# Kernel tuning notes

Measured on AMD Instinct MI355X. Metric: run time of the kernel, lower is better.

## Reference

```python
import jax, jax.numpy as jnp
import numpy as np
from jax import lax

K = 20
SLOPE = 0.01


def setup_inputs() -> dict:
    key = jax.random.key(0)
    k1, k2 = jax.random.split(key)
    x = jax.random.normal(k1, (8, 64, 4096), dtype=jnp.float32)
    # Conv2d(2*64, 64, kernel_size=1, bias=False) weight, squeezed to (out, in)
    W = jax.random.normal(k2, (64, 128), dtype=jnp.float32) * 0.05
    return {"x": x, "W": W}


def reference(x, W):
    # x: (B, C, N), W: (O, 2C)
    B, C, N = x.shape
    # --- knn: pairwise_distance[b,i,j] = -||x_i||^2 + 2 x_i.x_j - ||x_j||^2 ---
    xx = jnp.sum(x * x, axis=1)                      # (B, N)
    inner = jnp.einsum('bcn,bcm->bnm', x, x)         # (B, N, N)
    pdist = 2.0 * inner - xx[:, :, None] - xx[:, None, :]
    idx = lax.top_k(pdist, K)[1]                     # (B, N, K) neighbor indices
    # --- get_graph_feature: gather neighbors, diff + center concat ---
    x_t = jnp.transpose(x, (0, 2, 1))                # (B, N, C)
    neigh = x_t[jnp.arange(B)[:, None, None], idx]   # (B, N, K, C)
    center = x_t[:, :, None, :]                      # (B, N, 1, C)
    feat = jnp.concatenate(
        [neigh - center, jnp.broadcast_to(center, (B, N, K, C))], axis=-1
    )                                                # (B, N, K, 2C)
    # --- 1x1 conv (no bias) + LeakyReLU ---
    h = jnp.einsum('bnkd,od->bonk', feat, W)         # (B, O, N, K)
    h = jnp.where(h >= 0, h, SLOPE * h)
    # --- max over neighbors ---
    return jnp.max(h, axis=-1)                       # (B, O, N)
```

## Files before the change

### kernel.cpp

```cpp
#include <hip/hip_runtime.h>
#include <cfloat>

#define B_ 8
#define C_ 64
#define N_ 4096
#define K_ 20
#define MARGIN 0.08f
#define CAP 64

typedef float f32x4v  __attribute__((ext_vector_type(4)));
typedef float f32x16v __attribute__((ext_vector_type(16)));
typedef _Float16 f16x8 __attribute__((ext_vector_type(8)));
typedef unsigned long long u64;

#define OFF_IDX 131072
#define OFF_QG  2752512
#define OFF_P0  19529728
#define OFF_P1  23724032

__global__ __launch_bounds__(256) void k_split(const float* __restrict__ x,
                                               unsigned short* __restrict__ p0,
                                               unsigned short* __restrict__ p1,
                                               float* __restrict__ xxn) {
    int b = blockIdx.x & 7, mt = blockIdx.x >> 3;
    int m = mt * 256 + threadIdx.x;
    const float* xb = x + (size_t)b * C_ * N_;
    double ss = 0.0;
#pragma unroll 1
    for (int seg = 0; seg < 8; ++seg) {
        unsigned short h0[8], h1[8];
#pragma unroll
        for (int j = 0; j < 8; ++j) {
            float v = xb[(size_t)(seg * 8 + j) * N_ + m];
            ss += (double)v * (double)v;
            _Float16 a = (_Float16)v;
            float r = v - (float)a;
            _Float16 bq = (_Float16)(r * 4096.f);
            h0[j] = __builtin_bit_cast(unsigned short, a);
            h1[j] = __builtin_bit_cast(unsigned short, bq);
        }
        uint4 q0, q1;
        q0.x = h0[0] | (h0[1] << 16); q0.y = h0[2] | (h0[3] << 16);
        q0.z = h0[4] | (h0[5] << 16); q0.w = h0[6] | (h0[7] << 16);
        q1.x = h1[0] | (h1[1] << 16); q1.y = h1[2] | (h1[3] << 16);
        q1.z = h1[4] | (h1[5] << 16); q1.w = h1[6] | (h1[7] << 16);
        size_t o16 = (size_t)(b * 8 + seg) * N_ + m;
        ((uint4*)p0)[o16] = q0;
        ((uint4*)p1)[o16] = q1;
    }
    xxn[b * N_ + m] = (float)(-0.5 * ss);
}

__device__ __forceinline__ void score4(const char* sm, const float* xxs,
                                       int mlb, int mf, int h,
                                       const f16x8 b0[4], float s[16]) {
    f32x16v acc;
#pragma unroll
    for (int g2i = 0; g2i < 4; ++g2i) {
        f32x4v xv = *(const f32x4v*)&xxs[mlb + 4 * h + 8 * g2i];
#pragma unroll
        for (int q = 0; q < 4; ++q) acc[g2i * 4 + q] = xv[q];
    }
#pragma unroll
    for (int kc = 0; kc < 4; ++kc) {
        int seg = kc * 2 + h;
        f16x8 a0 = __builtin_bit_cast(f16x8,
            *(const f32x4v*)(sm + seg * 4096 + (mlb + mf) * 16));
        acc = __builtin_amdgcn_mfma_f32_32x32x16_f16(a0, b0[kc], acc, 0, 0, 0);
    }
#pragma unroll
    for (int r = 0; r < 16; ++r) s[r] = acc[r];
}

__device__ __forceinline__ void score16(const char* sm, const float* xxs,
                                        int mlb, int mf, int h,
                                        const f16x8 b0[4], const f16x8 b1[4],
                                        float s[16]) {
    const float c12 = 1.f / 4096.f;
    f32x16v acc1, acc2, acc3;
#pragma unroll
    for (int g2i = 0; g2i < 4; ++g2i) {
        f32x4v xv = *(const f32x4v*)&xxs[mlb + 4 * h + 8 * g2i];
#pragma unroll
        for (int q = 0; q < 4; ++q) {
            acc1[g2i * 4 + q] = xv[q];
            acc2[g2i * 4 + q] = 0.f;
            acc3[g2i * 4 + q] = 0.f;
        }
    }
#pragma unroll
    for (int kc = 0; kc < 4; ++kc) {
        int seg = kc * 2 + h;
        const char* pA = sm + seg * 4096 + (mlb + mf) * 16;
        f16x8 a0 = __builtin_bit_cast(f16x8, *(const f32x4v*)pA);
        f16x8 a1 = __builtin_bit_cast(f16x8, *(const f32x4v*)(pA + 32768));
        acc1 = __builtin_amdgcn_mfma_f32_32x32x16_f16(a0, b0[kc], acc1, 0, 0, 0);
        acc2 = __builtin_amdgcn_mfma_f32_32x32x16_f16(a0, b1[kc], acc2, 0, 0, 0);
        acc2 = __builtin_amdgcn_mfma_f32_32x32x16_f16(a1, b0[kc], acc2, 0, 0, 0);
        acc3 = __builtin_amdgcn_mfma_f32_32x32x16_f16(a1, b1[kc], acc3, 0, 0, 0);
    }
#pragma unroll
    for (int r = 0; r < 16; ++r)
        s[r] = acc1[r] + (acc2[r] + acc3[r] * c12) * c12;
}

__global__ __launch_bounds__(512, 4) void k_topk(const unsigned short* __restrict__ p0g,
                                                 const unsigned short* __restrict__ p1g,
                                                 const float* __restrict__ xxn,
                                                 u64* __restrict__ bufg,
                                                 int* __restrict__ idxo) {
    __shared__ __align__(16) char smem[67328];
    int b = blockIdx.x & 7, nt = blockIdx.x >> 3;
    int n0 = nt * 64;
    int tid = threadIdx.x;
    int w = tid >> 6, l = tid & 63, h = l >> 5, mf = l & 31;
    int cs = w >> 1, wg = w & 1;
    int rowl = wg * 32 + mf;
    int b8 = b * 8;
    const f32x4v* g0 = (const f32x4v*)p0g;
    const f32x4v* g1 = (const f32x4v*)p1g;
    float* Mp   = (float*)(smem + 32768);
    float* xxs  = (float*)(smem + 65792);
    int*   cntp = (int*)(smem + 66816);
    float* T2p  = (float*)(smem + 67072);

    f16x8 b0[4], b1[4];
#pragma unroll
    for (int kc = 0; kc < 4; ++kc) {
        int seg = kc * 2 + h;
        size_t gi = (size_t)(b8 + seg) * N_ + n0 + rowl;
        b0[kc] = __builtin_bit_cast(f16x8, g0[gi]);
        b1[kc] = __builtin_bit_cast(f16x8, g1[gi]);
    }

#pragma unroll 1
    for (int ch = 0; ch < 16; ++ch) {
        __syncthreads();
#pragma unroll
        for (int i = 0; i < 4; ++i) {
            int lin = i * 512 + tid;
            int seg = lin >> 8, ml = lin & 255;
            *(f32x4v*)(smem + seg * 4096 + ml * 16) =
                g0[(size_t)(b8 + seg) * N_ + ch * 256 + ml];
        }
        if (tid < 256) xxs[tid] = xxn[b * N_ + ch * 256 + tid];
        __syncthreads();
#pragma unroll
        for (int t = 0; t < 2; ++t) {
            int mlb = cs * 64 + t * 32;
            float s[16];
            score4(smem, xxs, mlb, mf, h, b0, s);
            float m8[8];
#pragma unroll
            for (int r = 0; r < 8; ++r) m8[r] = fmaxf(s[r], s[r + 8]);
            float mx = fmaxf(fmaxf(fmaxf(m8[0], m8[1]), fmaxf(m8[2], m8[3])),
                             fmaxf(fmaxf(m8[4], m8[5]), fmaxf(m8[6], m8[7])));
            mx = fmaxf(mx, __shfl_xor(mx, 32));
            if (l < 32)
                Mp[rowl * 129 + ch * 8 + t * 4 + cs] = mx;
        }
    }

    __syncthreads();
    if (tid < 256) {
        int row = tid >> 2, q = tid & 3;
        const float* mrow = Mp + row * 129 + q * 32;
        float v8[8];
#pragma unroll
        for (int j = 0; j < 8; ++j) v8[j] = -FLT_MAX;
#pragma unroll
        for (int i = 0; i < 32; ++i) {
            float v = mrow[i];
#pragma unroll
            for (int j = 7; j >= 1; --j) {
                bool c1 = v > v8[j - 1];
                float nv = c1 ? v8[j - 1] : v;
                v8[j] = (v > v8[j]) ? nv : v8[j];
            }
            v8[0] = fmaxf(v8[0], v);
        }
        float* lp = (float*)smem + row * 33 + q * 8;
#pragma unroll
        for (int j = 0; j < 8; ++j) lp[j] = v8[j];
    }
    __syncthreads();
    if (tid < 64) {
        const float* lp = (const float*)smem + tid * 33;
        float hv0 = lp[0], hv1 = lp[8], hv2 = lp[16], hv3 = lp[24];
        int p0 = 0, p1 = 0, p2 = 0, p3 = 0;
        float tstar = -FLT_MAX;
        for (int k = 0; k < 20; ++k) {
            bool a = hv0 >= hv1; float ma = a ? hv0 : hv1; int sa = a ? 0 : 1;
            bool bb = hv2 >= hv3; float mb = bb ? hv2 : hv3; int sb = bb ? 2 : 3;
            bool c = ma >= mb; tstar = c ? ma : mb; int sl = c ? sa : sb;
            if (sl == 0) { ++p0; hv0 = (p0 < 8) ? lp[p0] : -FLT_MAX; }
            else if (sl == 1) { ++p1; hv1 = (p1 < 8) ? lp[8 + p1] : -FLT_MAX; }
            else if (sl == 2) { ++p2; hv2 = (p2 < 8) ? lp[16 + p2] : -FLT_MAX; }
            else { ++p3; hv3 = (p3 < 8) ? lp[24 + p3] : -FLT_MAX; }
        }
        T2p[tid] = tstar - MARGIN;
        cntp[tid] = 0;
    }
    __syncthreads();
    float T2r = T2p[rowl];

#pragma unroll 1
    for (int ch = 0; ch < 16; ++ch) {
        __syncthreads();
#pragma unroll
        for (int i = 0; i < 8; ++i) {
            int lin = i * 512 + tid;
            int panel = lin >> 11;
            int rem = lin & 2047;
            int seg = rem >> 8, ml = rem & 255;
            size_t gi = (size_t)(b8 + seg) * N_ + ch * 256 + ml;
            const f32x4v* src = panel ? g1 : g0;
            *(f32x4v*)(smem + panel * 32768 + seg * 4096 + ml * 16) = src[gi];
        }
        if (tid < 256) xxs[tid] = xxn[b * N_ + ch * 256 + tid];
        __syncthreads();
#pragma unroll
        for (int t = 0; t < 2; ++t) {
            int mlb = cs * 64 + t * 32;
            float s[16];
            score16(smem, xxs, mlb, mf, h, b0, b1, s);
            unsigned msk = 0;
#pragma unroll
            for (int r = 0; r < 16; ++r) msk |= (s[r] >= T2r) ? (1u << r) : 0u;
            int cb = ch * 256 + mlb + 4 * h;
            while (msk) {
                int r = __ffs(msk) - 1;
                msk &= msk - 1;
                int cand = cb + (r & 3) + 8 * (r >> 2);
                float sv = s[r];
                unsigned sb = __float_as_uint(sv);
                unsigned kk = (sv < 0.f) ? ~sb : (sb | 0x80000000u);
                int slot = atomicAdd(cntp + rowl, 1);
                if (slot < CAP)
                    bufg[((size_t)(b * N_ + n0 + rowl)) * CAP + slot] =
                        ((u64)kk << 32) | (unsigned)(~cand);
            }
        }
    }

    __syncthreads();
    u64* keys = (u64*)smem;
#pragma unroll
    for (int i = 0; i < 8; ++i) {
        int p = i * 512 + tid;
        int row = p >> 6, slot = p & 63;
        int c_ = cntp[row]; c_ = (c_ > CAP) ? CAP : c_;
        u64 key = 0;
        if (slot < c_)
            key = bufg[((size_t)(b * N_ + n0 + row)) * CAP + slot];
        keys[row * (CAP + 1) + slot] = key;
    }
    __syncthreads();
    if (tid < 64) {
        int c_ = cntp[tid]; c_ = (c_ > CAP) ? CAP : c_;
        u64* kp = keys + tid * (CAP + 1);
        int* op = idxo + ((size_t)b * N_ + n0 + tid) * K_;
        for (int k = 0; k < K_; ++k) {
            u64 best = 0; int bs = 0;
            for (int s2 = 0; s2 < c_; ++s2) {
                bool g = kp[s2] > best;
                best = g ? kp[s2] : best;
                bs = g ? s2 : bs;
            }
            op[k] = (int)(~(unsigned)best) & 0xFFF;
            kp[bs] = 0;
        }
    }
}

__global__ __launch_bounds__(256) void k_qg(const float* __restrict__ x,
                                            const float* __restrict__ W,
                                            float* __restrict__ qg) {
    __shared__ float Wl[64 * 129];
    __shared__ float xs[64 * 64];
    int b = blockIdx.x & 7, mt = blockIdx.x >> 3;
    int mbase = mt * 64;
    int tid = threadIdx.x;

    for (int i = 0; i < 32; ++i) {
        int lin = tid + 256 * i;
        int c = lin & 63, o2 = lin >> 6;
        float wv;
        if (o2 < 64) wv = W[o2 * 128 + c];
        else { int o = o2 - 64; wv = W[o * 128 + 64 + c] - W[o * 128 + c]; }
        Wl[c * 129 + o2] = wv;
    }
#pragma unroll
    for (int i = 0; i < 4; ++i) {
        int lin = tid + 256 * i;
        int c = lin >> 4, f = lin & 15;
        *(float4*)&xs[c * 64 + f * 4] =
            *(const float4*)&x[((size_t)b * C_ + c) * N_ + mbase + f * 4];
    }
    __syncthreads();

    int u = tid & 63, half = tid >> 6;
    float a0[16], a1[16];
#pragma unroll
    for (int j = 0; j < 16; ++j) { a0[j] = 0.f; a1[j] = 0.f; }
#pragma unroll 4
    for (int c = 0; c < 64; ++c) {
        float2 wv = *(const float2*)&Wl[c * 129 + 2 * u];
        const float4* xr = (const float4*)&xs[c * 64 + half * 16];
        float4 v0 = xr[0], v1 = xr[1], v2 = xr[2], v3 = xr[3];
        float xvv[16];
        xvv[0]=v0.x; xvv[1]=v0.y; xvv[2]=v0.z; xvv[3]=v0.w;
        xvv[4]=v1.x; xvv[5]=v1.y; xvv[6]=v1.z; xvv[7]=v1.w;
        xvv[8]=v2.x; xvv[9]=v2.y; xvv[10]=v2.z; xvv[11]=v2.w;
        xvv[12]=v3.x; xvv[13]=v3.y; xvv[14]=v3.z; xvv[15]=v3.w;
#pragma unroll
        for (int j = 0; j < 16; ++j) { a0[j] += wv.x * xvv[j]; a1[j] += wv.y * xvv[j]; }
    }
#pragma unroll
    for (int j = 0; j < 16; ++j) {
        int m = mbase + half * 16 + j;
        float2 o; o.x = a0[j]; o.y = a1[j];
        *(float2*)&qg[((size_t)b * N_ + m) * 128 + 2 * u] = o;
    }
}

__global__ __launch_bounds__(256) void k_out(const float* __restrict__ qg,
                                             const int* __restrict__ idxi,
                                             float* __restrict__ out) {
    __shared__ float T[32][65];
    int b = blockIdx.x & 7, nt = blockIdx.x >> 3;
    int n0 = nt * 32;
    int tid = threadIdx.x;
    int w = tid >> 6, o = tid & 63;
    const float* qgb = qg + (size_t)b * N_ * 128;
    for (int i = 0; i < 8; ++i) {
        int nl = w * 8 + i;
        int n = n0 + nl;
        float gv = qgb[(size_t)n * 128 + 64 + o];
        const int* ip = idxi + ((size_t)b * N_ + n) * K_;
        float mx = -FLT_MAX;
#pragma unroll 5
        for (int k = 0; k < K_; ++k) {
            int ik = ip[k];
            float hh = qgb[(size_t)ik * 128 + o] + gv;
            hh = (hh >= 0.f) ? hh : 0.01f * hh;
            mx = fmaxf(mx, hh);
        }
        T[nl][o] = mx;
    }
    __syncthreads();
    int ow = tid >> 2, q = tid & 3;
#pragma unroll
    for (int j4 = 0; j4 < 2; ++j4) {
        int nl = q * 8 + j4 * 4;
        float4 v;
        v.x = T[nl + 0][ow]; v.y = T[nl + 1][ow];
        v.z = T[nl + 2][ow]; v.w = T[nl + 3][ow];
        *(float4*)&out[((size_t)b * 64 + ow) * N_ + n0 + nl] = v;
    }
}

extern "C" void kernel_launch(void* const* d_in, const int* in_sizes, int n_in,
                              void* d_out, int out_size, void* d_ws, size_t ws_size,
                              hipStream_t stream) {
    const float* x = (const float*)d_in[0];
    const float* W = (const float*)d_in[1];
    float* out = (float*)d_out;

    float*          xxn  = (float*)d_ws;
    int*            idx  = (int*)((char*)d_ws + OFF_IDX);
    float*          qg   = (float*)((char*)d_ws + OFF_QG);
    u64*            bufg = (u64*)((char*)d_ws + OFF_QG);
    unsigned short* p0   = (unsigned short*)((char*)d_ws + OFF_P0);
    unsigned short* p1   = (unsigned short*)((char*)d_ws + OFF_P1);

    k_split<<<dim3(128), dim3(256), 0, stream>>>(x, p0, p1, xxn);
    k_topk <<<dim3(512), dim3(512), 0, stream>>>(p0, p1, xxn, bufg, idx);
    k_qg   <<<dim3(512), dim3(256), 0, stream>>>(x, W, qg);
    k_out  <<<dim3(1024), dim3(256), 0, stream>>>(qg, idx, out);
}
```

Measured before the change: 253.4 us.

## Double-buffer key panels via direct global-to-LDS loads with explicit waitcnt barriers

Result: slower. 298.2 us (+17.6%).

```diff
diff --git a/kernel.cpp b/kernel.cpp
--- a/kernel.cpp
+++ b/kernel.cpp
@@ -17,6 +17,16 @@
 #define OFF_QG  2752512
 #define OFF_P0  19529728
 #define OFF_P1  23724032
+
+#define WAIT_VM(n) asm volatile("s_waitcnt vmcnt(" #n ")" ::: "memory")
+#define BAR_RAW()  asm volatile("s_barrier" ::: "memory")
+#define BAR_LDS()  asm volatile("s_waitcnt lgkmcnt(0)\n\ts_barrier" ::: "memory")
+
+__device__ __forceinline__ void gll16(const void* g, void* l) {
+    __builtin_amdgcn_global_load_lds(
+        (const __attribute__((address_space(1))) unsigned int*)g,
+        (__attribute__((address_space(3))) unsigned int*)l, 16, 0, 0);
+}
 
 __global__ __launch_bounds__(256) void k_split(const float* __restrict__ x,
                                                unsigned short* __restrict__ p0,
@@ -61,6 +71,7 @@
 #pragma unroll
         for (int q = 0; q < 4; ++q) acc[g2i * 4 + q] = xv[q];
     }
+    __builtin_amdgcn_s_setprio(1);
 #pragma unroll
     for (int kc = 0; kc < 4; ++kc) {
         int seg = kc * 2 + h;
@@ -68,6 +79,7 @@
             *(const f32x4v*)(sm + seg * 4096 + (mlb + mf) * 16));
         acc = __builtin_amdgcn_mfma_f32_32x32x16_f16(a0, b0[kc], acc, 0, 0, 0);
     }
+    __builtin_amdgcn_s_setprio(0);
 #pragma unroll
     for (int r = 0; r < 16; ++r) s[r] = acc[r];
 }
@@ -88,6 +100,7 @@
             acc3[g2i * 4 + q] = 0.f;
         }
     }
+    __builtin_amdgcn_s_setprio(1);
 #pragma unroll
     for (int kc = 0; kc < 4; ++kc) {
         int seg = kc * 2 + h;
@@ -99,30 +112,57 @@
         acc2 = __builtin_amdgcn_mfma_f32_32x32x16_f16(a1, b0[kc], acc2, 0, 0, 0);
         acc3 = __builtin_amdgcn_mfma_f32_32x32x16_f16(a1, b1[kc], acc3, 0, 0, 0);
     }
+    __builtin_amdgcn_s_setprio(0);
 #pragma unroll
     for (int r = 0; r < 16; ++r)
         s[r] = acc1[r] + (acc2[r] + acc3[r] * c12) * c12;
 }
 
-__global__ __launch_bounds__(512, 4) void k_topk(const unsigned short* __restrict__ p0g,
+__device__ __forceinline__ void stage1(char* smem, int bufoff, const f32x4v* g0,
+                                       int b8, int ch, int wq, int wr, int l) {
+#pragma unroll
+    for (int i = 0; i < 4; ++i) {
+        int seg = i * 2 + wq;
+        gll16(g0 + ((size_t)(b8 + seg) * N_ + ch * 256 + wr * 64 + l),
+              smem + bufoff + seg * 4096 + wr * 1024);
+    }
+}
+
+__device__ __forceinline__ void stage2(char* smem, int bufoff, const f32x4v* g0,
+                                       const f32x4v* g1, int b8, int ch,
+                                       int wq, int wr, int l) {
+#pragma unroll
+    for (int p = 0; p < 2; ++p) {
+        const f32x4v* g = p ? g1 : g0;
+#pragma unroll
+        for (int i = 0; i < 4; ++i) {
+            int seg = i * 2 + wq;
+            gll16(g + ((size_t)(b8 + seg) * N_ + ch * 256 + wr * 64 + l),
+                  smem + bufoff + p * 32768 + seg * 4096 + wr * 1024);
+        }
+    }
+}
+
+__global__ __launch_bounds__(512, 2) void k_topk(const unsigned short* __restrict__ p0g,
                                                  const unsigned short* __restrict__ p1g,
                                                  const float* __restrict__ xxn,
                                                  u64* __restrict__ bufg,
                                                  int* __restrict__ idxo) {
-    __shared__ __align__(16) char smem[67328];
+    __shared__ __align__(16) char smem[147968];
     int b = blockIdx.x & 7, nt = blockIdx.x >> 3;
     int n0 = nt * 64;
     int tid = threadIdx.x;
     int w = tid >> 6, l = tid & 63, h = l >> 5, mf = l & 31;
     int cs = w >> 1, wg = w & 1;
     int rowl = wg * 32 + mf;
+    int wq = w >> 2, wr = w & 3;
     int b8 = b * 8;
     const f32x4v* g0 = (const f32x4v*)p0g;
     const f32x4v* g1 = (const f32x4v*)p1g;
-    float* Mp   = (float*)(smem + 32768);
-    float* xxs  = (float*)(smem + 65792);
-    int*   cntp = (int*)(smem + 66816);
-    float* T2p  = (float*)(smem + 67072);
+    float* Mt   = (float*)(smem + 32768);
+    float* xxf  = (float*)(smem + 131072);
+    int*   cntp = (int*)(smem + 147456);
+    float* T2p  = (float*)(smem + 147712);
 
     f16x8 b0[4], b1[4];
 #pragma unroll
@@ -132,24 +172,31 @@
         b0[kc] = __builtin_bit_cast(f16x8, g0[gi]);
         b1[kc] = __builtin_bit_cast(f16x8, g1[gi]);
     }
-
+#pragma unroll
+    for (int i = 0; i < 2; ++i) {
+        int p = i * 512 + tid;
+        ((f32x4v*)xxf)[p] = ((const f32x4v*)(xxn + (size_t)b * N_))[p];
+    }
+    __syncthreads();
+
+    stage1(smem, 0, g0, b8, 0, wq, wr, l);
 #pragma unroll 1
     for (int ch = 0; ch < 16; ++ch) {
-        __syncthreads();
-#pragma unroll
-        for (int i = 0; i < 4; ++i) {
-            int lin = i * 512 + tid;
-            int seg = lin >> 8, ml = lin & 255;
-            *(f32x4v*)(smem + seg * 4096 + ml * 16) =
-                g0[(size_t)(b8 + seg) * N_ + ch * 256 + ml];
-        }
-        if (tid < 256) xxs[tid] = xxn[b * N_ + ch * 256 + tid];
-        __syncthreads();
+        int cur = (ch & 1) ? 65536 : 0;
+        if (ch < 15) {
+            stage1(smem, cur ^ 65536, g0, b8, ch + 1, wq, wr, l);
+            WAIT_VM(4);
+        } else {
+            WAIT_VM(0);
+        }
+        BAR_RAW();
+        const char* sm = smem + cur;
+        const float* xxs = xxf + ch * 256;
 #pragma unroll
         for (int t = 0; t < 2; ++t) {
             int mlb = cs * 64 + t * 32;
             float s[16];
-            score4(smem, xxs, mlb, mf, h, b0, s);
+            score4(sm, xxs, mlb, mf, h, b0, s);
             float m8[8];
 #pragma unroll
             for (int r = 0; r < 8; ++r) m8[r] = fmaxf(s[r], s[r + 8]);
@@ -157,20 +204,21 @@
                              fmaxf(fmaxf(m8[4], m8[5]), fmaxf(m8[6], m8[7])));
             mx = fmaxf(mx, __shfl_xor(mx, 32));
             if (l < 32)
-                Mp[rowl * 129 + ch * 8 + t * 4 + cs] = mx;
-        }
-    }
-
-    __syncthreads();
+                Mt[(ch * 8 + t * 4 + cs) * 64 + rowl] = mx;
+        }
+        BAR_RAW();
+    }
+
+    stage2(smem, 65536, g0, g1, b8, 0, wq, wr, l);
+    BAR_LDS();
     if (tid < 256) {
         int row = tid >> 2, q = tid & 3;
-        const float* mrow = Mp + row * 129 + q * 32;
         float v8[8];
 #pragma unroll
         for (int j = 0; j < 8; ++j) v8[j] = -FLT_MAX;
 #pragma unroll
         for (int i = 0; i < 32; ++i) {
-            float v = mrow[i];
+            float v = Mt[(q * 32 + i) * 64 + row];
 #pragma unroll
             for (int j = 7; j >= 1; --j) {
                 bool c1 = v > v8[j - 1];
@@ -183,7 +231,7 @@
 #pragma unroll
         for (int j = 0; j < 8; ++j) lp[j] = v8[j];
     }
-    __syncthreads();
+    BAR_LDS();
     if (tid < 64) {
         const float* lp = (const float*)smem + tid * 33;
         float hv0 = lp[0], hv1 = lp[8], hv2 = lp[16], hv3 = lp[24];
@@ -201,29 +249,26 @@
         T2p[tid] = tstar - MARGIN;
         cntp[tid] = 0;
     }
-    __syncthreads();
+    BAR_LDS();
     float T2r = T2p[rowl];
 
 #pragma unroll 1
     for (int ch = 0; ch < 16; ++ch) {
-        __syncthreads();
-#pragma unroll
-        for (int i = 0; i < 8; ++i) {
-            int lin = i * 512 + tid;
-            int panel = lin >> 11;
-            int rem = lin & 2047;
-            int seg = rem >> 8, ml = rem & 255;
-            size_t gi = (size_t)(b8 + seg) * N_ + ch * 256 + ml;
-            const f32x4v* src = panel ? g1 : g0;
-            *(f32x4v*)(smem + panel * 32768 + seg * 4096 + ml * 16) = src[gi];
-        }
-        if (tid < 256) xxs[tid] = xxn[b * N_ + ch * 256 + tid];
-        __syncthreads();
+        int cur = (ch & 1) ? 0 : 65536;
+        if (ch < 15) {
+            stage2(smem, cur ^ 65536, g0, g1, b8, ch + 1, wq, wr, l);
+            WAIT_VM(8);
+        } else {
+            WAIT_VM(0);
+        }
+        BAR_RAW();
+        const char* sm = smem + cur;
+        const float* xxs = xxf + ch * 256;
 #pragma unroll
         for (int t = 0; t < 2; ++t) {
             int mlb = cs * 64 + t * 32;
             float s[16];
-            score16(smem, xxs, mlb, mf, h, b0, b1, s);
+            score16(sm, xxs, mlb, mf, h, b0, b1, s);
             unsigned msk = 0;
 #pragma unroll
             for (int r = 0; r < 16; ++r) msk |= (s[r] >= T2r) ? (1u << r) : 0u;
@@ -241,6 +286,7 @@
                         ((u64)kk << 32) | (unsigned)(~cand);
             }
         }
+        BAR_RAW();
     }
 
     __syncthreads();
```
